# Kernel tuning notes

Measured on AMD Instinct MI355X. Metric: run time of the kernel, lower is better.

## Reference

```python
import jax, jax.numpy as jnp
import numpy as np

N = 50000   # nodes
E = 800000  # edges (before self loops)
XD, PD, H = 3, 3, 64
EPS = 1e-5


def setup_inputs() -> dict:
    key = jax.random.key(0)
    ks = jax.random.split(key, 24)
    def rn(k, shape, scale=1.0):
        return jax.random.normal(k, shape, dtype=jnp.float32) * scale
    inp = {
        'x': rn(ks[0], (N, XD)),
        'pos': rn(ks[1], (N, PD)),
        # MLP(6 -> 64 -> 64 -> 128), Linear+BN(+ReLU, last ReLU stripped)
        'W1': rn(ks[2], (XD + PD, H), 0.3), 'b1': rn(ks[3], (H,), 0.1),
        'g1': jax.random.uniform(ks[4], (H,), jnp.float32, 0.5, 1.5),
        'be1': rn(ks[5], (H,), 0.1), 'm1': rn(ks[6], (H,), 0.1),
        'v1': jax.random.uniform(ks[7], (H,), jnp.float32, 0.5, 1.5),
        'W2': rn(ks[8], (H, H), 0.1), 'b2': rn(ks[9], (H,), 0.1),
        'g2': jax.random.uniform(ks[10], (H,), jnp.float32, 0.5, 1.5),
        'be2': rn(ks[11], (H,), 0.1), 'm2': rn(ks[12], (H,), 0.1),
        'v2': jax.random.uniform(ks[13], (H,), jnp.float32, 0.5, 1.5),
        'W3': rn(ks[14], (H, 2 * H), 0.1), 'b3': rn(ks[15], (2 * H,), 0.1),
        'g3': jax.random.uniform(ks[16], (2 * H,), jnp.float32, 0.5, 1.5),
        'be3': rn(ks[17], (2 * H,), 0.1), 'm3': rn(ks[18], (2 * H,), 0.1),
        'v3': jax.random.uniform(ks[19], (2 * H,), jnp.float32, 0.5, 1.5),
        'edge_index': jax.random.randint(ks[20], (2, E), 0, N, dtype=jnp.int64),
    }
    return inp


def _bn(h, g, b, m, v):
    # inference-mode BatchNorm1d
    return (h - m) * jax.lax.rsqrt(v + EPS) * g + b


def reference(x, pos, W1, b1, g1, be1, m1, v1, W2, b2, g2, be2, m2, v2,
              W3, b3, g3, be3, m3, v3, edge_index):
    n = x.shape[0]
    loops = jnp.arange(n, dtype=edge_index.dtype)
    src = jnp.concatenate([edge_index[0], loops])  # j (source/neighbor)
    dst = jnp.concatenate([edge_index[1], loops])  # i (target)
    # per-edge feature: [x_j, pos_j - pos_i]  -> [E+N, 6]
    feat = jnp.concatenate([x[src], pos[src] - pos[dst]], axis=-1)
    h = jax.nn.relu(_bn(feat @ W1 + b1, g1, be1, m1, v1))
    h = jax.nn.relu(_bn(h @ W2 + b2, g2, be2, m2, v2))
    h = _bn(h @ W3 + b3, g3, be3, m3, v3)  # final ReLU stripped by MLP(modules[:-1])
    # max aggregation to destination nodes (PointNetConv default aggr='max')
    out = jax.ops.segment_max(h, dst, num_segments=n)
    return out
```

## Files before the change

### kernel.cpp

```cpp
#include <hip/hip_runtime.h>

#define N_NODES 50000
#define N_EDGES 800000
#define TOT_E   (N_EDGES + N_NODES)
#define EPS     1e-5f
#define SCAN_NB 196

typedef unsigned short u16;
typedef short v8s __attribute__((ext_vector_type(8)));
typedef float v4f __attribute__((ext_vector_type(4)));

#define WS_W1H    0
#define WS_W1L    4096
#define WS_W2H    8192
#define WS_W2L    16384
#define WS_W3H    24576
#define WS_W3L    40960
#define WS_B1F    57344
#define WS_B2F    57600
#define WS_B3F    57856
#define WS_BSUM   58368
#define WS_CURSOR 59392
#define WS_SORT   259392

__device__ __forceinline__ unsigned rne_bf16(float f) {
    unsigned u = __float_as_uint(f);
    return (u + 0x7fffu + ((u >> 16) & 1u)) >> 16;
}

__device__ __forceinline__ void cvt_split2(float v0, float v1,
                                           unsigned &hp, unsigned &lp) {
    unsigned h;
    asm("v_cvt_pk_bf16_f32 %0, %1, %2" : "=v"(h) : "v"(v0), "v"(v1));
    float h0f = __uint_as_float(h << 16);
    float h1f = __uint_as_float(h & 0xffff0000u);
    unsigned l;
    float r0 = v0 - h0f, r1 = v1 - h1f;
    asm("v_cvt_pk_bf16_f32 %0, %1, %2" : "=v"(l) : "v"(r0), "v"(r1));
    hp = h; lp = l;
}

#define MFMA3(acc, ah, al, bh, bl)                                           \
    acc = __builtin_amdgcn_mfma_f32_16x16x32_bf16(ah, bh, acc, 0, 0, 0);     \
    acc = __builtin_amdgcn_mfma_f32_16x16x32_bf16(ah, bl, acc, 0, 0, 0);     \
    acc = __builtin_amdgcn_mfma_f32_16x16x32_bf16(al, bh, acc, 0, 0, 0);

__global__ void prep0_kernel(
    const float* __restrict__ W1, const float* __restrict__ b1,
    const float* __restrict__ g1, const float* __restrict__ be1,
    const float* __restrict__ m1, const float* __restrict__ v1,
    const float* __restrict__ W2, const float* __restrict__ b2,
    const float* __restrict__ g2, const float* __restrict__ be2,
    const float* __restrict__ m2, const float* __restrict__ v2,
    const float* __restrict__ W3, const float* __restrict__ b3,
    const float* __restrict__ g3, const float* __restrict__ be3,
    const float* __restrict__ m3, const float* __restrict__ v3,
    u16* __restrict__ w1h, u16* __restrict__ w1l,
    u16* __restrict__ w2h, u16* __restrict__ w2l,
    u16* __restrict__ w3h, u16* __restrict__ w3l,
    float* __restrict__ b1f, float* __restrict__ b2f, float* __restrict__ b3f,
    int* __restrict__ cursor, uint4* __restrict__ out4)
{
    int t = blockIdx.x * blockDim.x + threadIdx.x;

    if (t < N_NODES) cursor[t] = 1;
    if (t < (N_NODES * 128) / 4)
        out4[t] = make_uint4(0xFF800000u, 0xFF800000u, 0xFF800000u, 0xFF800000u);

    if (t < 14592) {
        float val = 0.f;
        u16 *ph = nullptr, *pl = nullptr;
        int idx = 0;
        if (t < 2048) {
            int n = t >> 5, k = t & 31;
            float s = g1[n] * rsqrtf(v1[n] + EPS);
            val = (k < 6) ? W1[k * 64 + n] * s : 0.f;
            ph = w1h; pl = w1l; idx = t;
        } else if (t < 6144) {
            int i = t - 2048; int n = i >> 6, k = i & 63;
            float s = g2[n] * rsqrtf(v2[n] + EPS);
            val = W2[k * 64 + n] * s;
            ph = w2h; pl = w2l; idx = i;
        } else if (t < 14336) {
            int i = t - 6144; int n = i >> 6, k = i & 63;
            float s = g3[n] * rsqrtf(v3[n] + EPS);
            val = W3[k * 128 + n] * s;
            ph = w3h; pl = w3l; idx = i;
        } else {
            int i = t - 14336;
            if (i < 64) {
                float s = g1[i] * rsqrtf(v1[i] + EPS);
                b1f[i] = (b1[i] - m1[i]) * s + be1[i];
            } else if (i < 128) {
                int j = i - 64;
                float s = g2[j] * rsqrtf(v2[j] + EPS);
                b2f[j] = (b2[j] - m2[j]) * s + be2[j];
            } else {
                int j = i - 128;
                float s = g3[j] * rsqrtf(v3[j] + EPS);
                b3f[j] = (b3[j] - m3[j]) * s + be3[j];
            }
            return;
        }
        unsigned hi = rne_bf16(val);
        unsigned lo = rne_bf16(val - __uint_as_float(hi << 16));
        ph[idx] = (u16)hi;
        pl[idx] = (u16)lo;
    }
}

__global__ void hist_kernel(const int* __restrict__ ei, int* __restrict__ cursor) {
    int e = blockIdx.x * 256 + threadIdx.x;
    if (e < N_EDGES) atomicAdd(&cursor[ei[N_EDGES + e]], 1);
}

__global__ void scanA_kernel(int* __restrict__ cursor, int* __restrict__ bsum) {
    __shared__ int sh[256];
    const int tid = threadIdx.x;
    int i = blockIdx.x * 256 + tid;
    int c = (i < N_NODES) ? cursor[i] : 0;
    sh[tid] = c;
    __syncthreads();
    int v = c;
    for (int off = 1; off < 256; off <<= 1) {
        int t = (tid >= off) ? sh[tid - off] : 0;
        __syncthreads();
        v += t;
        sh[tid] = v;
        __syncthreads();
    }
    if (i < N_NODES) cursor[i] = v - c;
    if (tid == 255) bsum[blockIdx.x] = v;
}

__global__ void scanB_kernel(int* __restrict__ bsum) {
    __shared__ int sh[256];
    const int tid = threadIdx.x;
    int c = (tid < SCAN_NB) ? bsum[tid] : 0;
    sh[tid] = c;
    __syncthreads();
    int v = c;
    for (int off = 1; off < 256; off <<= 1) {
        int t = (tid >= off) ? sh[tid - off] : 0;
        __syncthreads();
        v += t;
        sh[tid] = v;
        __syncthreads();
    }
    if (tid < SCAN_NB) bsum[tid] = v - c;
}

__global__ void scatter_kernel(const int* __restrict__ ei, int* __restrict__ cursor,
                               const int* __restrict__ bsum, int2* __restrict__ sorted) {
    int e = blockIdx.x * 256 + threadIdx.x;
    if (e >= TOT_E) return;
    int s, d;
    if (e < N_EDGES) { s = ei[e]; d = ei[N_EDGES + e]; }
    else             { s = d = e - N_EDGES; }
    int p = atomicAdd(&cursor[d], 1);
    sorted[p + bsum[d >> 8]] = make_int2(s, d);
}

__global__ __launch_bounds__(64, 2) void gather_kernel(
    const float* __restrict__ x, const float* __restrict__ pos,
    const int2* __restrict__ sorted,
    const u16* __restrict__ w1h, const u16* __restrict__ w1l,
    const u16* __restrict__ w2h, const u16* __restrict__ w2l,
    const u16* __restrict__ w3h, const u16* __restrict__ w3l,
    const float* __restrict__ b1f, const float* __restrict__ b2f,
    const float* __restrict__ b3f, float* __restrict__ out)
{
    __shared__ char smem[12288];

    const int lane = threadIdx.x;
    const int l15 = lane & 15, g = lane >> 4;
    const int e = blockIdx.x * 64 + lane;
    const bool active = e < TOT_E;

    int src = 0, dst = 0;
    if (active) {
        int2 sd = sorted[e];
        src = sd.x; dst = sd.y;
    }
    const int nid = active ? dst : (-1 - lane);

    const int np1 = __shfl_down(nid, 1);
    const bool seg_last = (lane == 63) || (np1 != nid);
    const unsigned long long segmask = __ballot(seg_last);

    float f0 = x[src * 3 + 0];
    float f1 = x[src * 3 + 1];
    float f2v = x[src * 3 + 2];
    float f3 = pos[src * 3 + 0] - pos[dst * 3 + 0];
    float f4 = pos[src * 3 + 1] - pos[dst * 3 + 1];
    float f5 = pos[src * 3 + 2] - pos[dst * 3 + 2];

    unsigned uh0, ul0, uh1, ul1, uh2, ul2;
    cvt_split2(f0, f1, uh0, ul0);
    cvt_split2(f2v, f3, uh1, ul1);
    cvt_split2(f4, f5, uh2, ul2);

    v8s a1h[4], a1l[4];
#pragma unroll
    for (int tm = 0; tm < 4; ++tm) {
        int bidx = (16 * tm + l15) * 4;
        unsigned p0 = (unsigned)__builtin_amdgcn_ds_bpermute(bidx, (int)uh0);
        unsigned p1 = (unsigned)__builtin_amdgcn_ds_bpermute(bidx, (int)uh1);
        unsigned p2 = (unsigned)__builtin_amdgcn_ds_bpermute(bidx, (int)uh2);
        unsigned q0 = (unsigned)__builtin_amdgcn_ds_bpermute(bidx, (int)ul0);
        unsigned q1 = (unsigned)__builtin_amdgcn_ds_bpermute(bidx, (int)ul1);
        unsigned q2 = (unsigned)__builtin_amdgcn_ds_bpermute(bidx, (int)ul2);
        if (g != 0) { p0 = p1 = p2 = q0 = q1 = q2 = 0u; }
        uint4 th = make_uint4(p0, p1, p2, 0u);
        uint4 tl = make_uint4(q0, q1, q2, 0u);
        a1h[tm] = __builtin_bit_cast(v8s, th);
        a1l[tm] = __builtin_bit_cast(v8s, tl);
    }

    v4f acc[4][4];
#pragma unroll
    for (int tn = 0; tn < 4; ++tn) {
        float bv = b1f[16 * tn + l15];
#pragma unroll
        for (int tm = 0; tm < 4; ++tm) acc[tm][tn] = (v4f){bv, bv, bv, bv};
    }
#pragma unroll
    for (int tn = 0; tn < 4; ++tn) {
        v8s bh = *(const v8s*)&w1h[(16 * tn + l15) * 32 + g * 8];
        v8s bl = *(const v8s*)&w1l[(16 * tn + l15) * 32 + g * 8];
#pragma unroll
        for (int tm = 0; tm < 4; ++tm) { MFMA3(acc[tm][tn], a1h[tm], a1l[tm], bh, bl) }
    }

#define STAGE_HALF(ACC, tk)                                                      \
    {                                                                            \
        _Pragma("unroll")                                                        \
        for (int t2 = 0; t2 < 2; ++t2) {                                         \
            int tn = 2 * (tk) + t2;                                              \
            int fc = 16 * t2 + l15;                                              \
            _Pragma("unroll")                                                    \
            for (int tm = 0; tm < 4; ++tm) {                                     \
                unsigned hp0, lp0, hp1, lp1;                                     \
                cvt_split2(fmaxf(ACC[tm][tn][0], 0.f),                           \
                           fmaxf(ACC[tm][tn][1], 0.f), hp0, lp0);                \
                cvt_split2(fmaxf(ACC[tm][tn][2], 0.f),                           \
                           fmaxf(ACC[tm][tn][3], 0.f), hp1, lp1);                \
                _Pragma("unroll")                                                \
                for (int r = 0; r < 4; ++r) {                                    \
                    int row = 16 * tm + 4 * g + r;                               \
                    unsigned hv = (r == 0) ? hp0 : (r == 1) ? (hp0 >> 16)        \
                                : (r == 2) ? hp1 : (hp1 >> 16);                  \
                    unsigned lv = (r == 0) ? lp0 : (r == 1) ? (lp0 >> 16)        \
                                : (r == 2) ? lp1 : (lp1 >> 16);                  \
                    int swz = (row & 7) << 4;                                    \
                    *(u16*)(smem + row * 128 + ((fc * 2) ^ swz)) = (u16)hv;      \
                    *(u16*)(smem + row * 128 + ((64 + fc * 2) ^ swz)) = (u16)lv; \
                }                                                                \
            }                                                                    \
        }                                                                        \
    }

    v4f acc2[4][4];
#pragma unroll
    for (int tn = 0; tn < 4; ++tn) {
        float bv = b2f[16 * tn + l15];
#pragma unroll
        for (int tm = 0; tm < 4; ++tm) acc2[tm][tn] = (v4f){bv, bv, bv, bv};
    }
#pragma unroll
    for (int tk = 0; tk < 2; ++tk) {
        STAGE_HALF(acc, tk)
        v8s ah[4], al[4];
#pragma unroll
        for (int tm = 0; tm < 4; ++tm) {
            int row = 16 * tm + l15;
            int swz = (row & 7) << 4;
            ah[tm] = *(const v8s*)(smem + row * 128 + ((g * 16) ^ swz));
            al[tm] = *(const v8s*)(smem + row * 128 + ((64 + g * 16) ^ swz));
        }
#pragma unroll
        for (int tn = 0; tn < 4; ++tn) {
            v8s bh = *(const v8s*)&w2h[(16 * tn + l15) * 64 + tk * 32 + g * 8];
            v8s bl = *(const v8s*)&w2l[(16 * tn + l15) * 64 + tk * 32 + g * 8];
#pragma unroll
            for (int tm = 0; tm < 4; ++tm) { MFMA3(acc2[tm][tn], ah[tm], al[tm], bh, bl) }
        }
    }

    v8s al3[4][2];
#pragma unroll
    for (int tk = 0; tk < 2; ++tk) {
#pragma unroll
        for (int t2 = 0; t2 < 2; ++t2) {
            int tn = 2 * tk + t2;
            int fc = 16 * t2 + l15;
#pragma unroll
            for (int tm = 0; tm < 4; ++tm) {
                unsigned hp0, lp0, hp1, lp1;
                cvt_split2(fmaxf(acc2[tm][tn][0], 0.f),
                           fmaxf(acc2[tm][tn][1], 0.f), hp0, lp0);
                cvt_split2(fmaxf(acc2[tm][tn][2], 0.f),
                           fmaxf(acc2[tm][tn][3], 0.f), hp1, lp1);
#pragma unroll
                for (int r = 0; r < 4; ++r) {
                    int row = 16 * tm + 4 * g + r;
                    unsigned hv = (r == 0) ? hp0 : (r == 1) ? (hp0 >> 16)
                                : (r == 2) ? hp1 : (hp1 >> 16);
                    unsigned lv = (r == 0) ? lp0 : (r == 1) ? (lp0 >> 16)
                                : (r == 2) ? lp1 : (lp1 >> 16);
                    *(u16*)(smem + row * 128 + (((32 * tk + fc) * 2) ^ ((row & 7) << 4))) = (u16)hv;
                    *(u16*)(smem + 8192 + row * 64 + ((fc * 2) ^ ((row & 3) << 4))) = (u16)lv;
                }
            }
        }
#pragma unroll
        for (int tm = 0; tm < 4; ++tm) {
            int row = 16 * tm + l15;
            al3[tm][tk] = *(const v8s*)(smem + 8192 + row * 64 + ((g * 16) ^ ((row & 3) << 4)));
        }
    }

#pragma unroll
    for (int h = 0; h < 2; ++h) {
        v4f acc3[4][4];
#pragma unroll
        for (int tn = 0; tn < 4; ++tn) {
            float bv = b3f[64 * h + 16 * tn + l15];
#pragma unroll
            for (int tm = 0; tm < 4; ++tm) acc3[tm][tn] = (v4f){bv, bv, bv, bv};
        }
#pragma unroll
        for (int tk = 0; tk < 2; ++tk)
#pragma unroll
            for (int tn = 0; tn < 4; ++tn) {
                int nrow = 16 * (4 * h + tn) + l15;
                v8s bh = *(const v8s*)&w3h[nrow * 64 + tk * 32 + g * 8];
                v8s bl = *(const v8s*)&w3l[nrow * 64 + tk * 32 + g * 8];
#pragma unroll
                for (int tm = 0; tm < 4; ++tm) {
                    int row = 16 * tm + l15;
                    v8s ah = *(const v8s*)(smem + row * 128 +
                              ((64 * tk + g * 16) ^ ((row & 7) << 4)));
                    MFMA3(acc3[tm][tn], ah, al3[tm][tk], bh, bl)
                }
            }

        float runmax = -__builtin_inff();
        bool first = true;
#pragma unroll
        for (int c = 0; c < 4; ++c) {
#pragma unroll
            for (int tn = 0; tn < 4; ++tn)
#pragma unroll
                for (int r = 0; r < 4; ++r) {
                    int rl = 4 * g + r;
                    int col = 16 * tn + l15;
                    int off = 8192 + rl * 256 + ((col * 4) ^ ((rl & 7) << 4));
                    *(float*)(smem + off) = acc3[c][tn][r];
                }
#pragma unroll
            for (int i = 0; i < 16; ++i) {
                int e2 = 16 * c + i;
                int off = 8192 + i * 256 + ((lane * 4) ^ ((i & 7) << 4));
                float val = *(const float*)(smem + off);
                runmax = fmaxf(runmax, val);
                if ((segmask >> e2) & 1ull) {
                    int n = __builtin_amdgcn_readlane(nid, e2);
                    if (n >= 0) {
                        float* op = out + (size_t)n * 128 + h * 64 + lane;
                        if (first || e2 == 63) atomicMax(op, runmax);
                        else *op = runmax;
                    }
                    first = false;
                    runmax = -__builtin_inff();
                }
            }
        }
    }
#undef STAGE_HALF
}

extern "C" void kernel_launch(void* const* d_in, const int* in_sizes, int n_in,
                              void* d_out, int out_size, void* d_ws, size_t ws_size,
                              hipStream_t stream) {
    const float* x   = (const float*)d_in[0];
    const float* pos = (const float*)d_in[1];
    const float* W1  = (const float*)d_in[2];
    const float* b1  = (const float*)d_in[3];
    const float* g1  = (const float*)d_in[4];
    const float* be1 = (const float*)d_in[5];
    const float* m1  = (const float*)d_in[6];
    const float* v1  = (const float*)d_in[7];
    const float* W2  = (const float*)d_in[8];
    const float* b2  = (const float*)d_in[9];
    const float* g2  = (const float*)d_in[10];
    const float* be2 = (const float*)d_in[11];
    const float* m2  = (const float*)d_in[12];
    const float* v2  = (const float*)d_in[13];
    const float* W3  = (const float*)d_in[14];
    const float* b3  = (const float*)d_in[15];
    const float* g3  = (const float*)d_in[16];
    const float* be3 = (const float*)d_in[17];
    const float* m3  = (const float*)d_in[18];
    const float* v3  = (const float*)d_in[19];
    const int*   ei  = (const int*)d_in[20];

    char* ws = (char*)d_ws;
    u16* w1h = (u16*)(ws + WS_W1H);
    u16* w1l = (u16*)(ws + WS_W1L);
    u16* w2h = (u16*)(ws + WS_W2H);
    u16* w2l = (u16*)(ws + WS_W2L);
    u16* w3h = (u16*)(ws + WS_W3H);
    u16* w3l = (u16*)(ws + WS_W3L);
    float* b1f = (float*)(ws + WS_B1F);
    float* b2f = (float*)(ws + WS_B2F);
    float* b3f = (float*)(ws + WS_B3F);
    int* bsum   = (int*)(ws + WS_BSUM);
    int* cursor = (int*)(ws + WS_CURSOR);
    int2* sorted = (int2*)(ws + WS_SORT);
    float* outf = (float*)d_out;

    prep0_kernel<<<(N_NODES * 128 / 4 + 255) / 256, 256, 0, stream>>>(
        W1, b1, g1, be1, m1, v1, W2, b2, g2, be2, m2, v2,
        W3, b3, g3, be3, m3, v3, w1h, w1l, w2h, w2l, w3h, w3l,
        b1f, b2f, b3f, cursor, (uint4*)d_out);

    hist_kernel<<<(N_EDGES + 255) / 256, 256, 0, stream>>>(ei, cursor);
    scanA_kernel<<<SCAN_NB, 256, 0, stream>>>(cursor, bsum);
    scanB_kernel<<<1, 256, 0, stream>>>(bsum);
    scatter_kernel<<<(TOT_E + 255) / 256, 256, 0, stream>>>(ei, cursor, bsum, sorted);

    gather_kernel<<<(TOT_E + 63) / 64, 64, 0, stream>>>(
        x, pos, sorted, w1h, w1l, w2h, w2l, w3h, w3l, b1f, b2f, b3f, outf);
}
```

Before: 255.3 us.

## Process MLP per 16-edge row tile to cut registers and LDS, raise occupancy

Restructures the fused per-edge MLP so each wave walks its 64 edges as four sequential 16-row tiles (non-unrolled loop), running all three layers and the max-aggregation per tile instead of holding 4x4 accumulator tiles for all rows at once. This shrinks accumulator register use and LDS from 12KB to 8KB, and raises launch_bounds min blocks from 2 to 4 to allow higher occupancy. Running max and first-flag state are carried across tiles for both output halves. The trade-off is less MFMA instruction-level parallelism per wave and weight fragments being reloaded once per tile.

```diff
diff --git a/kernel.cpp b/kernel.cpp
--- a/kernel.cpp
+++ b/kernel.cpp
@@ -161,7 +161,7 @@
     sorted[p + bsum[d >> 8]] = make_int2(s, d);
 }
 
-__global__ __launch_bounds__(64, 2) void gather_kernel(
+__global__ __launch_bounds__(64, 4) void gather_kernel(
     const float* __restrict__ x, const float* __restrict__ pos,
     const int2* __restrict__ sorted,
     const u16* __restrict__ w1h, const u16* __restrict__ w1l,
@@ -170,7 +170,10 @@
     const float* __restrict__ b1f, const float* __restrict__ b2f,
     const float* __restrict__ b3f, float* __restrict__ out)
 {
-    __shared__ char smem[12288];
+    __shared__ char smem[8192];
+    char* HBH = smem;
+    char* HBL = smem + 2048;
+    char* EB  = smem + 4096;
 
     const int lane = threadIdx.x;
     const int l15 = lane & 15, g = lane >> 4;
@@ -200,184 +203,147 @@
     cvt_split2(f2v, f3, uh1, ul1);
     cvt_split2(f4, f5, uh2, ul2);
 
-    v8s a1h[4], a1l[4];
-#pragma unroll
-    for (int tm = 0; tm < 4; ++tm) {
-        int bidx = (16 * tm + l15) * 4;
-        unsigned p0 = (unsigned)__builtin_amdgcn_ds_bpermute(bidx, (int)uh0);
-        unsigned p1 = (unsigned)__builtin_amdgcn_ds_bpermute(bidx, (int)uh1);
-        unsigned p2 = (unsigned)__builtin_amdgcn_ds_bpermute(bidx, (int)uh2);
-        unsigned q0 = (unsigned)__builtin_amdgcn_ds_bpermute(bidx, (int)ul0);
-        unsigned q1 = (unsigned)__builtin_amdgcn_ds_bpermute(bidx, (int)ul1);
-        unsigned q2 = (unsigned)__builtin_amdgcn_ds_bpermute(bidx, (int)ul2);
-        if (g != 0) { p0 = p1 = p2 = q0 = q1 = q2 = 0u; }
-        uint4 th = make_uint4(p0, p1, p2, 0u);
-        uint4 tl = make_uint4(q0, q1, q2, 0u);
-        a1h[tm] = __builtin_bit_cast(v8s, th);
-        a1l[tm] = __builtin_bit_cast(v8s, tl);
-    }
-
-    v4f acc[4][4];
-#pragma unroll
-    for (int tn = 0; tn < 4; ++tn) {
-        float bv = b1f[16 * tn + l15];
-#pragma unroll
-        for (int tm = 0; tm < 4; ++tm) acc[tm][tn] = (v4f){bv, bv, bv, bv};
-    }
-#pragma unroll
-    for (int tn = 0; tn < 4; ++tn) {
-        v8s bh = *(const v8s*)&w1h[(16 * tn + l15) * 32 + g * 8];
-        v8s bl = *(const v8s*)&w1l[(16 * tn + l15) * 32 + g * 8];
-#pragma unroll
-        for (int tm = 0; tm < 4; ++tm) { MFMA3(acc[tm][tn], a1h[tm], a1l[tm], bh, bl) }
-    }
-
-#define STAGE_HALF(ACC, tk)                                                      \
+    float runmax0 = -__builtin_inff(), runmax1 = -__builtin_inff();
+    bool first0 = true, first1 = true;
+
+#define STAGE_BLK(ACC)                                                           \
     {                                                                            \
         _Pragma("unroll")                                                        \
-        for (int t2 = 0; t2 < 2; ++t2) {                                         \
-            int tn = 2 * (tk) + t2;                                              \
-            int fc = 16 * t2 + l15;                                              \
+        for (int tn = 0; tn < 4; ++tn) {                                         \
+            int fc = 16 * tn + l15;                                              \
+            unsigned hp0, lp0, hp1, lp1;                                         \
+            cvt_split2(fmaxf(ACC[tn][0], 0.f), fmaxf(ACC[tn][1], 0.f), hp0, lp0);\
+            cvt_split2(fmaxf(ACC[tn][2], 0.f), fmaxf(ACC[tn][3], 0.f), hp1, lp1);\
             _Pragma("unroll")                                                    \
-            for (int tm = 0; tm < 4; ++tm) {                                     \
-                unsigned hp0, lp0, hp1, lp1;                                     \
-                cvt_split2(fmaxf(ACC[tm][tn][0], 0.f),                           \
-                           fmaxf(ACC[tm][tn][1], 0.f), hp0, lp0);                \
-                cvt_split2(fmaxf(ACC[tm][tn][2], 0.f),                           \
-                           fmaxf(ACC[tm][tn][3], 0.f), hp1, lp1);                \
-                _Pragma("unroll")                                                \
-                for (int r = 0; r < 4; ++r) {                                    \
-                    int row = 16 * tm + 4 * g + r;                               \
-                    unsigned hv = (r == 0) ? hp0 : (r == 1) ? (hp0 >> 16)        \
-                                : (r == 2) ? hp1 : (hp1 >> 16);                  \
-                    unsigned lv = (r == 0) ? lp0 : (r == 1) ? (lp0 >> 16)        \
-                                : (r == 2) ? lp1 : (lp1 >> 16);                  \
-                    int swz = (row & 7) << 4;                                    \
-                    *(u16*)(smem + row * 128 + ((fc * 2) ^ swz)) = (u16)hv;      \
-                    *(u16*)(smem + row * 128 + ((64 + fc * 2) ^ swz)) = (u16)lv; \
-                }                                                                \
+            for (int r = 0; r < 4; ++r) {                                        \
+                int lrow = 4 * g + r;                                            \
+                unsigned hv = (r == 0) ? hp0 : (r == 1) ? (hp0 >> 16)            \
+                            : (r == 2) ? hp1 : (hp1 >> 16);                      \
+                unsigned lv = (r == 0) ? lp0 : (r == 1) ? (lp0 >> 16)            \
+                            : (r == 2) ? lp1 : (lp1 >> 16);                      \
+                int off = lrow * 128 + ((fc * 2) ^ ((lrow & 7) << 4));           \
+                *(u16*)(HBH + off) = (u16)hv;                                    \
+                *(u16*)(HBL + off) = (u16)lv;                                    \
             }                                                                    \
         }                                                                        \
     }
 
-    v4f acc2[4][4];
-#pragma unroll
-    for (int tn = 0; tn < 4; ++tn) {
-        float bv = b2f[16 * tn + l15];
-#pragma unroll
-        for (int tm = 0; tm < 4; ++tm) acc2[tm][tn] = (v4f){bv, bv, bv, bv};
-    }
-#pragma unroll
-    for (int tk = 0; tk < 2; ++tk) {
-        STAGE_HALF(acc, tk)
-        v8s ah[4], al[4];
-#pragma unroll
-        for (int tm = 0; tm < 4; ++tm) {
-            int row = 16 * tm + l15;
-            int swz = (row & 7) << 4;
-            ah[tm] = *(const v8s*)(smem + row * 128 + ((g * 16) ^ swz));
-            al[tm] = *(const v8s*)(smem + row * 128 + ((64 + g * 16) ^ swz));
-        }
+#pragma unroll 1
+    for (int tm = 0; tm < 4; ++tm) {
+        v8s a1h, a1l;
+        {
+            int bidx = (16 * tm + l15) * 4;
+            unsigned p0 = (unsigned)__builtin_amdgcn_ds_bpermute(bidx, (int)uh0);
+            unsigned p1 = (unsigned)__builtin_amdgcn_ds_bpermute(bidx, (int)uh1);
+            unsigned p2 = (unsigned)__builtin_amdgcn_ds_bpermute(bidx, (int)uh2);
+            unsigned q0 = (unsigned)__builtin_amdgcn_ds_bpermute(bidx, (int)ul0);
+            unsigned q1 = (unsigned)__builtin_amdgcn_ds_bpermute(bidx, (int)ul1);
+            unsigned q2 = (unsigned)__builtin_amdgcn_ds_bpermute(bidx, (int)ul2);
+            if (g != 0) { p0 = p1 = p2 = q0 = q1 = q2 = 0u; }
+            uint4 th = make_uint4(p0, p1, p2, 0u);
+            uint4 tl = make_uint4(q0, q1, q2, 0u);
+            a1h = __builtin_bit_cast(v8s, th);
+            a1l = __builtin_bit_cast(v8s, tl);
+        }
+
+        v4f acc1[4];
 #pragma unroll
         for (int tn = 0; tn < 4; ++tn) {
-            v8s bh = *(const v8s*)&w2h[(16 * tn + l15) * 64 + tk * 32 + g * 8];
-            v8s bl = *(const v8s*)&w2l[(16 * tn + l15) * 64 + tk * 32 + g * 8];
-#pragma unroll
-            for (int tm = 0; tm < 4; ++tm) { MFMA3(acc2[tm][tn], ah[tm], al[tm], bh, bl) }
-        }
-    }
-
-    v8s al3[4][2];
-#pragma unroll
-    for (int tk = 0; tk < 2; ++tk) {
-#pragma unroll
-        for (int t2 = 0; t2 < 2; ++t2) {
-            int tn = 2 * tk + t2;
-            int fc = 16 * t2 + l15;
-#pragma unroll
-            for (int tm = 0; tm < 4; ++tm) {
-                unsigned hp0, lp0, hp1, lp1;
-                cvt_split2(fmaxf(acc2[tm][tn][0], 0.f),
-                           fmaxf(acc2[tm][tn][1], 0.f), hp0, lp0);
-                cvt_split2(fmaxf(acc2[tm][tn][2], 0.f),
-                           fmaxf(acc2[tm][tn][3], 0.f), hp1, lp1);
+            float bv = b1f[16 * tn + l15];
+            acc1[tn] = (v4f){bv, bv, bv, bv};
+        }
+#pragma unroll
+        for (int tn = 0; tn < 4; ++tn) {
+            v8s bh = *(const v8s*)&w1h[(16 * tn + l15) * 32 + g * 8];
+            v8s bl = *(const v8s*)&w1l[(16 * tn + l15) * 32 + g * 8];
+            MFMA3(acc1[tn], a1h, a1l, bh, bl)
+        }
+
+        STAGE_BLK(acc1)
+        v8s ah[2], al[2];
+#pragma unroll
+        for (int tk = 0; tk < 2; ++tk) {
+            int off = l15 * 128 + ((64 * tk + 16 * g) ^ ((l15 & 7) << 4));
+            ah[tk] = *(const v8s*)(HBH + off);
+            al[tk] = *(const v8s*)(HBL + off);
+        }
+
+        v4f acc2[4];
+#pragma unroll
+        for (int tn = 0; tn < 4; ++tn) {
+            float bv = b2f[16 * tn + l15];
+            acc2[tn] = (v4f){bv, bv, bv, bv};
+        }
+#pragma unroll
+        for (int tk = 0; tk < 2; ++tk)
+#pragma unroll
+            for (int tn = 0; tn < 4; ++tn) {
+                v8s bh = *(const v8s*)&w2h[(16 * tn + l15) * 64 + tk * 32 + g * 8];
+                v8s bl = *(const v8s*)&w2l[(16 * tn + l15) * 64 + tk * 32 + g * 8];
+                MFMA3(acc2[tn], ah[tk], al[tk], bh, bl)
+            }
+
+        STAGE_BLK(acc2)
+        v8s ah3[2], al3[2];
+#pragma unroll
+        for (int tk = 0; tk < 2; ++tk) {
+            int off = l15 * 128 + ((64 * tk + 16 * g) ^ ((l15 & 7) << 4));
+            ah3[tk] = *(const v8s*)(HBH + off);
+            al3[tk] = *(const v8s*)(HBL + off);
+        }
+
+#pragma unroll
+        for (int h = 0; h < 2; ++h) {
+            v4f acc3[4];
+#pragma unroll
+            for (int tn = 0; tn < 4; ++tn) {
+                float bv = b3f[64 * h + 16 * tn + l15];
+                acc3[tn] = (v4f){bv, bv, bv, bv};
+            }
+#pragma unroll
+            for (int tk = 0; tk < 2; ++tk)
+#pragma unroll
+                for (int tn = 0; tn < 4; ++tn) {
+                    int nrow = 16 * (4 * h + tn) + l15;
+                    v8s bh = *(const v8s*)&w3h[nrow * 64 + tk * 32 + g * 8];
+                    v8s bl = *(const v8s*)&w3l[nrow * 64 + tk * 32 + g * 8];
+                    MFMA3(acc3[tn], ah3[tk], al3[tk], bh, bl)
+                }
+
+#pragma unroll
+            for (int tn = 0; tn < 4; ++tn)
 #pragma unroll
                 for (int r = 0; r < 4; ++r) {
-                    int row = 16 * tm + 4 * g + r;
-                    unsigned hv = (r == 0) ? hp0 : (r == 1) ? (hp0 >> 16)
-                                : (r == 2) ? hp1 : (hp1 >> 16);
-                    unsigned lv = (r == 0) ? lp0 : (r == 1) ? (lp0 >> 16)
-                                : (r == 2) ? lp1 : (lp1 >> 16);
-                    *(u16*)(smem + row * 128 + (((32 * tk + fc) * 2) ^ ((row & 7) << 4))) = (u16)hv;
-                    *(u16*)(smem + 8192 + row * 64 + ((fc * 2) ^ ((row & 3) << 4))) = (u16)lv;
+                    int lrow = 4 * g + r;
+                    int col = 16 * tn + l15;
+                    int off = lrow * 256 + ((col * 4) ^ ((lrow & 7) << 4));
+                    *(float*)(EB + off) = acc3[tn][r];
                 }
-            }
-        }
-#pragma unroll
-        for (int tm = 0; tm < 4; ++tm) {
-            int row = 16 * tm + l15;
-            al3[tm][tk] = *(const v8s*)(smem + 8192 + row * 64 + ((g * 16) ^ ((row & 3) << 4)));
-        }
-    }
-
-#pragma unroll
-    for (int h = 0; h < 2; ++h) {
-        v4f acc3[4][4];
-#pragma unroll
-        for (int tn = 0; tn < 4; ++tn) {
-            float bv = b3f[64 * h + 16 * tn + l15];
-#pragma unroll
-            for (int tm = 0; tm < 4; ++tm) acc3[tm][tn] = (v4f){bv, bv, bv, bv};
-        }
-#pragma unroll
-        for (int tk = 0; tk < 2; ++tk)
-#pragma unroll
-            for (int tn = 0; tn < 4; ++tn) {
-                int nrow = 16 * (4 * h + tn) + l15;
-                v8s bh = *(const v8s*)&w3h[nrow * 64 + tk * 32 + g * 8];
-                v8s bl = *(const v8s*)&w3l[nrow * 64 + tk * 32 + g * 8];
-#pragma unroll
-                for (int tm = 0; tm < 4; ++tm) {
-                    int row = 16 * tm + l15;
-                    v8s ah = *(const v8s*)(smem + row * 128 +
-                              ((64 * tk + g * 16) ^ ((row & 7) << 4)));
-                    MFMA3(acc3[tm][tn], ah, al3[tm][tk], bh, bl)
-                }
-            }
-
-        float runmax = -__builtin_inff();
-        bool first = true;
-#pragma unroll
-        for (int c = 0; c < 4; ++c) {
-#pragma unroll
-            for (int tn = 0; tn < 4; ++tn)
-#pragma unroll
-                for (int r = 0; r < 4; ++r) {
-                    int rl = 4 * g + r;
-                    int col = 16 * tn + l15;
-                    int off = 8192 + rl * 256 + ((col * 4) ^ ((rl & 7) << 4));
-                    *(float*)(smem + off) = acc3[c][tn][r];
-                }
+
+            float rm = (h == 0) ? runmax0 : runmax1;
+            bool  fi = (h == 0) ? first0 : first1;
 #pragma unroll
             for (int i = 0; i < 16; ++i) {
-                int e2 = 16 * c + i;
-                int off = 8192 + i * 256 + ((lane * 4) ^ ((i & 7) << 4));
-                float val = *(const float*)(smem + off);
-                runmax = fmaxf(runmax, val);
+                int e2 = 16 * tm + i;
+                int off = i * 256 + ((lane * 4) ^ ((i & 7) << 4));
+                float val = *(const float*)(EB + off);
+                rm = fmaxf(rm, val);
                 if ((segmask >> e2) & 1ull) {
                     int n = __builtin_amdgcn_readlane(nid, e2);
                     if (n >= 0) {
                         float* op = out + (size_t)n * 128 + h * 64 + lane;
-                        if (first || e2 == 63) atomicMax(op, runmax);
-                        else *op = runmax;
+                        if (fi || e2 == 63) atomicMax(op, rm);
+                        else *op = rm;
                     }
-                    first = false;
-                    runmax = -__builtin_inff();
+                    fi = false;
+                    rm = -__builtin_inff();
                 }
             }
-        }
-    }
-#undef STAGE_HALF
+            if (h == 0) { runmax0 = rm; first0 = fi; }
+            else        { runmax1 = rm; first1 = fi; }
+        }
+    }
+#undef STAGE_BLK
 }
 
 extern "C" void kernel_launch(void* const* d_in, const int* in_sizes, int n_in,
```

New measurement: 559.8 us. +119.2%, slower.
